# Optimization experiments

Hardware: AMD Instinct MI355X
Metric: run time of the kernel (lower is better)

Reference implementation:

```python
import jax, jax.numpy as jnp
import numpy as np

N_HEADS = 8
EMBED = 640
CROSS = 768
HEAD = EMBED // N_HEADS


def setup_inputs() -> dict:
    key = jax.random.key(0)
    ks = jax.random.split(key, 10)
    s_e = 1.0 / np.sqrt(EMBED)
    s_c = 1.0 / np.sqrt(CROSS)
    return {
        "x": jax.random.normal(ks[0], (8, 4096, EMBED), jnp.float32),
        "y": jax.random.normal(ks[1], (8, 77, CROSS), jnp.float32),
        "Wq": jax.random.uniform(ks[2], (EMBED, EMBED), jnp.float32, -s_e, s_e),
        "bq": jax.random.uniform(ks[3], (EMBED,), jnp.float32, -s_e, s_e),
        "Wk": jax.random.uniform(ks[4], (CROSS, EMBED), jnp.float32, -s_c, s_c),
        "bk": jax.random.uniform(ks[5], (EMBED,), jnp.float32, -s_c, s_c),
        "Wv": jax.random.uniform(ks[6], (CROSS, EMBED), jnp.float32, -s_c, s_c),
        "bv": jax.random.uniform(ks[7], (EMBED,), jnp.float32, -s_c, s_c),
        "Wo": jax.random.uniform(ks[8], (EMBED, EMBED), jnp.float32, -s_e, s_e),
        "bo": jax.random.uniform(ks[9], (EMBED,), jnp.float32, -s_e, s_e),
    }


def reference(x, y, Wq, bq, Wk, bk, Wv, bv, Wo, bo):
    B, T, C = x.shape
    S = y.shape[1]
    # projections; split heads: [B, H, T, D]
    q = (x @ Wq + bq).reshape(B, T, N_HEADS, HEAD).transpose(0, 2, 1, 3)
    k = (y @ Wk + bk).reshape(B, S, N_HEADS, HEAD).transpose(0, 2, 1, 3)
    v = (y @ Wv + bv).reshape(B, S, N_HEADS, HEAD).transpose(0, 2, 1, 3)
    scores = jnp.einsum("bhtd,bhsd->bhts", q, k) / jnp.sqrt(jnp.float32(HEAD))
    attn = jax.nn.softmax(scores, axis=-1)
    out = jnp.einsum("bhts,bhsd->bhtd", attn, v)
    out = out.transpose(0, 2, 1, 3).reshape(B, T, C)
    return out @ Wo + bo
```

## Files before the change

kernel.cpp:

```cpp
#include <hip/hip_runtime.h>
#include <hip/hip_bf16.h>
#include <hip/hip_fp16.h>

#define EMBED 640
#define CROSS 768
#define NH 8
#define HEAD 80
#define BATCH 8
#define SEQT 4096
#define SEQS 77
#define MROWS (BATCH * SEQT)

typedef _Float16 half8 __attribute__((ext_vector_type(8)));
typedef float floatx4 __attribute__((ext_vector_type(4)));

__device__ __forceinline__ void lds_load16(const void* g, void* l) {
    __builtin_amdgcn_global_load_lds(
        (const __attribute__((address_space(1))) void*)g,
        (__attribute__((address_space(3))) void*)l, 16, 0, 0);
}

__global__ __launch_bounds__(256) void cvt_f32_f16(
    const float* __restrict__ in, _Float16* __restrict__ out)
{
    size_t i = ((size_t)blockIdx.x * 256 + threadIdx.x) * 8;
    float4 a = *(const float4*)&in[i];
    float4 b = *(const float4*)&in[i + 4];
    half8 h;
    h[0] = (_Float16)a.x; h[1] = (_Float16)a.y;
    h[2] = (_Float16)a.z; h[3] = (_Float16)a.w;
    h[4] = (_Float16)b.x; h[5] = (_Float16)b.y;
    h[6] = (_Float16)b.z; h[7] = (_Float16)b.w;
    *(half8*)&out[i] = h;
}

__global__ __launch_bounds__(256) void cvt_y_f16(
    const float* __restrict__ y, _Float16* __restrict__ yh)
{
    size_t i = ((size_t)blockIdx.x * 256 + threadIdx.x) * 8;
    half8 h = {};
    if (i < (size_t)BATCH * SEQS * CROSS) {
        float4 a = *(const float4*)&y[i];
        float4 b = *(const float4*)&y[i + 4];
        h[0] = (_Float16)a.x; h[1] = (_Float16)a.y;
        h[2] = (_Float16)a.z; h[3] = (_Float16)a.w;
        h[4] = (_Float16)b.x; h[5] = (_Float16)b.y;
        h[6] = (_Float16)b.z; h[7] = (_Float16)b.w;
    }
    *(half8*)&yh[i] = h;
}

__global__ __launch_bounds__(256) void zero_f16(_Float16* __restrict__ p, size_t n8)
{
    size_t i = (size_t)blockIdx.x * 256 + threadIdx.x;
    if (i < n8) *(half8*)&p[i * 8] = (half8){};
}

__global__ __launch_bounds__(256) void transpose_cvt(
    const float* __restrict__ W, _Float16* __restrict__ Wt, int K, int N)
{
    __shared__ float t[32][33];
    const int k0 = blockIdx.y * 32, n0 = blockIdx.x * 32;
    for (int r = threadIdx.y; r < 32; r += 8)
        t[r][threadIdx.x] = W[(size_t)(k0 + r) * N + n0 + threadIdx.x];
    __syncthreads();
    for (int r = threadIdx.y; r < 32; r += 8)
        Wt[(size_t)(n0 + r) * K + k0 + threadIdx.x] = (_Float16)t[threadIdx.x][r];
}

template <bool HALF_OUT>
__global__ __launch_bounds__(256) void gemm_f16(
    const _Float16* __restrict__ A,
    const _Float16* __restrict__ Bt,
    const float* __restrict__ bias,
    void* __restrict__ Cout, int M, int N, int K, float scale)
{
    __shared__ _Float16 As[3][128 * 32];
    __shared__ _Float16 Bs[3][128 * 32];

    const int tid  = threadIdx.x;
    const int wave = tid >> 6;
    const int lane = tid & 63;
    const int quad = lane >> 4;
    const int l16  = lane & 15;

    const int l   = blockIdx.y * gridDim.x + blockIdx.x;
    const int inner = l >> 3;
    const int p   = (l & 7) + 8 * (inner / gridDim.x);
    const int nt  = inner % gridDim.x;
    const int m0 = p * 128, n0 = nt * 128;
    const int wm = (wave >> 1) * 64, wn = (wave & 1) * 64;

    const int row = tid >> 2;
    const int kch = ((tid & 3) ^ ((row >> 1) & 3)) * 8;
    const int cq  = (quad ^ ((l16 >> 1) & 3)) * 8;

    const _Float16* pa0 = &A [(size_t)(m0 + row)      * K + kch];
    const _Float16* pa1 = &A [(size_t)(m0 + 64 + row) * K + kch];
    const _Float16* pb0 = &Bt[(size_t)(n0 + row)      * K + kch];
    const _Float16* pb1 = &Bt[(size_t)(n0 + 64 + row) * K + kch];

    const int NT = K / 32;

    auto stage = [&](int t) {
        const int bf = t % 3;
        const int off = t * 32;
        lds_load16(pa0 + off, &As[bf][wave * 512]);
        lds_load16(pa1 + off, &As[bf][2048 + wave * 512]);
        lds_load16(pb0 + off, &Bs[bf][wave * 512]);
        lds_load16(pb1 + off, &Bs[bf][2048 + wave * 512]);
    };
    stage(0); stage(1); stage(2);

    floatx4 acc[4][4] = {};

    for (int t = 0; t < NT; ++t) {
        const int rem = NT - 1 - t;
        if (rem >= 2)      asm volatile("s_waitcnt vmcnt(8)" ::: "memory");
        else if (rem == 1) asm volatile("s_waitcnt vmcnt(4)" ::: "memory");
        else               asm volatile("s_waitcnt vmcnt(0)" ::: "memory");
        __builtin_amdgcn_s_barrier();

        const _Float16* as = As[t % 3];
        const _Float16* bs = Bs[t % 3];
        half8 a[4], b[4];
        #pragma unroll
        for (int i = 0; i < 4; ++i)
            a[i] = *(const half8*)&as[(wm + i * 16 + l16) * 32 + cq];
        #pragma unroll
        for (int j = 0; j < 4; ++j)
            b[j] = *(const half8*)&bs[(wn + j * 16 + l16) * 32 + cq];
        #pragma unroll
        for (int i = 0; i < 4; ++i)
            #pragma unroll
            for (int j = 0; j < 4; ++j)
                acc[i][j] = __builtin_amdgcn_mfma_f32_16x16x32_f16(
                    a[i], b[j], acc[i][j], 0, 0, 0);

        asm volatile("s_waitcnt lgkmcnt(0)" ::: "memory");
        __builtin_amdgcn_s_barrier();
        if (t + 3 < NT) stage(t + 3);
    }

    float bcol[4];
    #pragma unroll
    for (int j = 0; j < 4; ++j) bcol[j] = bias[n0 + wn + j * 16 + l16];
    #pragma unroll
    for (int i = 0; i < 4; ++i)
        #pragma unroll
        for (int r = 0; r < 4; ++r) {
            const int m = m0 + wm + i * 16 + quad * 4 + r;
            #pragma unroll
            for (int j = 0; j < 4; ++j) {
                float v = (acc[i][j][r] + bcol[j]) * scale;
                const size_t off = (size_t)m * N + n0 + wn + j * 16 + l16;
                if (HALF_OUT) ((_Float16*)Cout)[off] = (_Float16)v;
                else          ((float*)Cout)[off] = v;
            }
        }
}

__global__ __launch_bounds__(256) void kv_gemm(
    const _Float16* __restrict__ yh,
    const _Float16* __restrict__ Wkt, const _Float16* __restrict__ Wvt,
    const float* __restrict__ bk, const float* __restrict__ bv,
    _Float16* __restrict__ kh, _Float16* __restrict__ vth)
{
    __shared__ _Float16 As[64 * 32];
    __shared__ _Float16 Bs[64 * 32];

    const int tid = threadIdx.x;
    const int wave = tid >> 6, lane = tid & 63;
    const int quad = lane >> 4, l16 = lane & 15;
    const int m0 = blockIdx.y * 64, n0 = blockIdx.x * 64;
    const bool isV = blockIdx.z != 0;
    const _Float16* Bt = isV ? Wvt : Wkt;
    const float* bias  = isV ? bv : bk;

    const int row = tid >> 2;
    const int kch = (tid & 3) * 8;

    floatx4 acc[4] = {};

    for (int k0 = 0; k0 < CROSS; k0 += 32) {
        lds_load16(&yh[(size_t)(m0 + row) * CROSS + k0 + kch], &As[wave * 512]);
        lds_load16(&Bt[(size_t)(n0 + row) * CROSS + k0 + kch], &Bs[wave * 512]);
        __syncthreads();
        half8 b = *(const half8*)&Bs[(wave * 16 + l16) * 32 + quad * 8];
        #pragma unroll
        for (int i = 0; i < 4; ++i) {
            half8 a = *(const half8*)&As[(i * 16 + l16) * 32 + quad * 8];
            acc[i] = __builtin_amdgcn_mfma_f32_16x16x32_f16(a, b, acc[i], 0, 0, 0);
        }
        __syncthreads();
    }

    const int n = n0 + wave * 16 + l16;
    const int h = n / HEAD, d = n % HEAD;
    const float bb = bias[n];
    #pragma unroll
    for (int i = 0; i < 4; ++i)
        #pragma unroll
        for (int r = 0; r < 4; ++r) {
            const int m = m0 + i * 16 + quad * 4 + r;
            if (m >= BATCH * SEQS) continue;
            const int b_ = m / SEQS, s = m % SEQS;
            const int bh = b_ * NH + h;
            const float v = acc[i][r] + bb;
            if (isV) vth[(size_t)bh * (HEAD * 80) + d * 80 + s] = (_Float16)v;
            else     kh [(size_t)bh * (SEQS * HEAD) + s * HEAD + d] = (_Float16)v;
        }
}

__global__ __launch_bounds__(256, 4) void attn_mfma(
    const _Float16* __restrict__ qh,
    const _Float16* __restrict__ kh,
    const _Float16* __restrict__ vth,
    _Float16* __restrict__ oh)
{
    constexpr int LS = 88;
    __shared__ _Float16 lds[(80 + 80 + 64) * LS + 8];
    _Float16* Ks = lds;
    _Float16* Vt = lds + 80 * LS;
    _Float16* Ps = lds + 160 * LS;

    const int tid = threadIdx.x;
    const int wave = tid >> 6, lane = tid & 63;
    const int quad = lane >> 4, l16 = lane & 15;
    const int bh = blockIdx.y;
    const int b = bh >> 3, h = bh & 7;
    const size_t row0 = (size_t)b * SEQT + (size_t)blockIdx.x * 256;
    const half8 hz = {};

    const _Float16* qp = qh + (row0 + wave * 16 + l16) * EMBED + h * HEAD;

    half8 qa0 = *(const half8*)&qp[quad * 8];
    half8 qa1 = *(const half8*)&qp[32 + quad * 8];
    half8 qa2 = (quad < 2) ? *(const half8*)&qp[64 + quad * 8] : hz;

    for (int idx = tid; idx < 80 * 11; idx += 256) {
        const int s = idx / 11, c = idx % 11;
        half8 v = hz;
        if (s < SEQS && c < 10)
            v = *(const half8*)&kh[(size_t)bh * (SEQS * HEAD) + s * HEAD + c * 8];
        *(half8*)&Ks[s * LS + c * 8] = v;
    }
    for (int idx = tid; idx < 80 * 11; idx += 256) {
        const int d = idx / 11, c = idx % 11;
        half8 v = hz;
        if (c < 10)
            v = *(const half8*)&vth[(size_t)bh * (HEAD * 80) + d * 80 + c * 8];
        *(half8*)&Vt[d * LS + c * 8] = v;
    }
    __syncthreads();

    for (int t = 0; t < 4; ++t) {
        floatx4 accs[5] = {};
        #pragma unroll
        for (int st = 0; st < 5; ++st) {
            const _Float16* kr = &Ks[(st * 16 + l16) * LS];
            half8 b0 = *(const half8*)&kr[quad * 8];
            half8 b1 = *(const half8*)&kr[32 + quad * 8];
            half8 b2 = *(const half8*)&kr[64 + quad * 8];
            accs[st] = __builtin_amdgcn_mfma_f32_16x16x32_f16(qa0, b0, accs[st], 0, 0, 0);
            accs[st] = __builtin_amdgcn_mfma_f32_16x16x32_f16(qa1, b1, accs[st], 0, 0, 0);
            accs[st] = __builtin_amdgcn_mfma_f32_16x16x32_f16(qa2, b2, accs[st], 0, 0, 0);
        }
        if (l16 >= 13) {
            accs[4][0] = -1e30f; accs[4][1] = -1e30f;
            accs[4][2] = -1e30f; accs[4][3] = -1e30f;
        }

        float recip[4];
        #pragma unroll
        for (int r = 0; r < 4; ++r) {
            float m = accs[0][r];
            #pragma unroll
            for (int st = 1; st < 5; ++st) m = fmaxf(m, accs[st][r]);
            m = fmaxf(m, __shfl_xor(m, 1));
            m = fmaxf(m, __shfl_xor(m, 2));
            m = fmaxf(m, __shfl_xor(m, 4));
            m = fmaxf(m, __shfl_xor(m, 8));
            float l = 0.f;
            const int row = wave * 16 + quad * 4 + r;
            #pragma unroll
            for (int st = 0; st < 5; ++st) {
                float e = __expf(accs[st][r] - m);
                l += e;
                Ps[row * LS + st * 16 + l16] = (_Float16)e;
            }
            l += __shfl_xor(l, 1);
            l += __shfl_xor(l, 2);
            l += __shfl_xor(l, 4);
            l += __shfl_xor(l, 8);
            recip[r] = 1.0f / l;
        }
        __syncthreads();

        half8 qn0 = hz, qn1 = hz, qn2 = hz;
        if (t < 3) {
            const _Float16* qn = qp + (size_t)(t + 1) * 64 * EMBED;
            qn0 = *(const half8*)&qn[quad * 8];
            qn1 = *(const half8*)&qn[32 + quad * 8];
            if (quad < 2) qn2 = *(const half8*)&qn[64 + quad * 8];
        }

        const _Float16* pr = &Ps[(wave * 16 + l16) * LS];
        half8 pa0 = *(const half8*)&pr[quad * 8];
        half8 pa1 = *(const half8*)&pr[32 + quad * 8];
        half8 pa2 = (quad < 2) ? *(const half8*)&pr[64 + quad * 8] : hz;
        __syncthreads();

        floatx4 acco[5] = {};
        #pragma unroll
        for (int dt = 0; dt < 5; ++dt) {
            const _Float16* vr = &Vt[(dt * 16 + l16) * LS];
            half8 b0 = *(const half8*)&vr[quad * 8];
            half8 b1 = *(const half8*)&vr[32 + quad * 8];
            half8 b2 = *(const half8*)&vr[64 + quad * 8];
            acco[dt] = __builtin_amdgcn_mfma_f32_16x16x32_f16(pa0, b0, acco[dt], 0, 0, 0);
            acco[dt] = __builtin_amdgcn_mfma_f32_16x16x32_f16(pa1, b1, acco[dt], 0, 0, 0);
            acco[dt] = __builtin_amdgcn_mfma_f32_16x16x32_f16(pa2, b2, acco[dt], 0, 0, 0);
        }

        #pragma unroll
        for (int r = 0; r < 4; ++r) {
            const size_t grow = row0 + t * 64 + wave * 16 + quad * 4 + r;
            #pragma unroll
            for (int dt = 0; dt < 5; ++dt)
                oh[grow * EMBED + h * HEAD + dt * 16 + l16] =
                    (_Float16)(acco[dt][r] * recip[r]);
        }

        qa0 = qn0; qa1 = qn1; qa2 = qn2;
    }
}

extern "C" void kernel_launch(void* const* d_in, const int* in_sizes, int n_in,
                              void* d_out, int out_size, void* d_ws, size_t ws_size,
                              hipStream_t stream)
{
    const float* x  = (const float*)d_in[0];
    const float* y  = (const float*)d_in[1];
    const float* Wq = (const float*)d_in[2];
    const float* bq = (const float*)d_in[3];
    const float* Wk = (const float*)d_in[4];
    const float* bk = (const float*)d_in[5];
    const float* Wv = (const float*)d_in[6];
    const float* bv = (const float*)d_in[7];
    const float* Wo = (const float*)d_in[8];
    const float* bo = (const float*)d_in[9];
    float* out = (float*)d_out;

    const size_t ME = (size_t)MROWS * EMBED;
    _Float16* xh  = (_Float16*)d_ws;
    _Float16* qh  = xh + ME;
    _Float16* ah  = qh + ME;
    _Float16* kh  = ah + ME;
    _Float16* vth = kh  + (size_t)BATCH * NH * SEQS * HEAD;
    _Float16* wqt = vth + (size_t)BATCH * NH * HEAD * 80;
    _Float16* wot = wqt + (size_t)EMBED * EMBED;
    _Float16* yh  = wot + (size_t)EMBED * EMBED;
    _Float16* wkt = yh  + (size_t)640 * CROSS;
    _Float16* wvt = wkt + (size_t)EMBED * CROSS;

    cvt_f32_f16<<<dim3(ME / (256 * 8)), 256, 0, stream>>>(x, xh);
    transpose_cvt<<<dim3(EMBED / 32, EMBED / 32), dim3(32, 8), 0, stream>>>(Wq, wqt, EMBED, EMBED);
    transpose_cvt<<<dim3(EMBED / 32, EMBED / 32), dim3(32, 8), 0, stream>>>(Wo, wot, EMBED, EMBED);
    transpose_cvt<<<dim3(EMBED / 32, CROSS / 32), dim3(32, 8), 0, stream>>>(Wk, wkt, CROSS, EMBED);
    transpose_cvt<<<dim3(EMBED / 32, CROSS / 32), dim3(32, 8), 0, stream>>>(Wv, wvt, CROSS, EMBED);
    cvt_y_f16<<<dim3(640 * CROSS / (256 * 8)), 256, 0, stream>>>(y, yh);
    zero_f16<<<dim3(((size_t)BATCH * NH * HEAD * 80 / 8 + 255) / 256), 256, 0, stream>>>(
        vth, (size_t)BATCH * NH * HEAD * 80 / 8);

    gemm_f16<true><<<dim3(EMBED / 128, MROWS / 128), 256, 0, stream>>>(
        xh, wqt, bq, qh, MROWS, EMBED, EMBED, 0.11180339887498949f);
    kv_gemm<<<dim3(EMBED / 64, 640 / 64, 2), 256, 0, stream>>>(
        yh, wkt, wvt, bk, bv, kh, vth);
    attn_mfma<<<dim3(SEQT / 256, BATCH * NH), 256, 0, stream>>>(qh, kh, vth, ah);
    gemm_f16<false><<<dim3(EMBED / 128, MROWS / 128), 256, 0, stream>>>(
        ah, wot, bo, out, MROWS, EMBED, EMBED, 1.0f);
}
```

Baseline: 301.2 us.

## Merge setup kernels and use single-barrier prefetch pipeline in GEMM

Folds the four weight transposes into one launch indexed by blockIdx.z, and combines the y conversion with zeroing of the V buffer into another. This cuts the number of small kernel launches. The GEMM main loop now uses a prefetch depth of two and issues the next stage right after a single barrier, dropping the second barrier and lgkmcnt wait per iteration. The risk is less memory latency hiding with the shallower prefetch, and possible races if the three-buffer rotation does not fully protect a buffer still being read.

```diff
diff --git a/kernel.cpp b/kernel.cpp
--- a/kernel.cpp
+++ b/kernel.cpp
@@ -34,38 +34,50 @@
     *(half8*)&out[i] = h;
 }
 
-__global__ __launch_bounds__(256) void cvt_y_f16(
-    const float* __restrict__ y, _Float16* __restrict__ yh)
-{
-    size_t i = ((size_t)blockIdx.x * 256 + threadIdx.x) * 8;
-    half8 h = {};
-    if (i < (size_t)BATCH * SEQS * CROSS) {
-        float4 a = *(const float4*)&y[i];
-        float4 b = *(const float4*)&y[i + 4];
-        h[0] = (_Float16)a.x; h[1] = (_Float16)a.y;
-        h[2] = (_Float16)a.z; h[3] = (_Float16)a.w;
-        h[4] = (_Float16)b.x; h[5] = (_Float16)b.y;
-        h[6] = (_Float16)b.z; h[7] = (_Float16)b.w;
-    }
-    *(half8*)&yh[i] = h;
-}
-
-__global__ __launch_bounds__(256) void zero_f16(_Float16* __restrict__ p, size_t n8)
-{
-    size_t i = (size_t)blockIdx.x * 256 + threadIdx.x;
-    if (i < n8) *(half8*)&p[i * 8] = (half8){};
-}
-
-__global__ __launch_bounds__(256) void transpose_cvt(
-    const float* __restrict__ W, _Float16* __restrict__ Wt, int K, int N)
+__global__ __launch_bounds__(256) void transpose_all(
+    const float* __restrict__ Wq, const float* __restrict__ Wo,
+    const float* __restrict__ Wk, const float* __restrict__ Wv,
+    _Float16* __restrict__ wqt, _Float16* __restrict__ wot,
+    _Float16* __restrict__ wkt, _Float16* __restrict__ wvt)
 {
     __shared__ float t[32][33];
+    const int z = blockIdx.z;
+    const float* W;  _Float16* Wt;  int K;
+    if      (z == 0) { W = Wq; Wt = wqt; K = EMBED; }
+    else if (z == 1) { W = Wo; Wt = wot; K = EMBED; }
+    else if (z == 2) { W = Wk; Wt = wkt; K = CROSS; }
+    else             { W = Wv; Wt = wvt; K = CROSS; }
+    const int N = EMBED;
     const int k0 = blockIdx.y * 32, n0 = blockIdx.x * 32;
+    if (k0 >= K) return;
     for (int r = threadIdx.y; r < 32; r += 8)
         t[r][threadIdx.x] = W[(size_t)(k0 + r) * N + n0 + threadIdx.x];
     __syncthreads();
     for (int r = threadIdx.y; r < 32; r += 8)
         Wt[(size_t)(n0 + r) * K + k0 + threadIdx.x] = (_Float16)t[threadIdx.x][r];
+}
+
+__global__ __launch_bounds__(256) void cvt_y_zero(
+    const float* __restrict__ y, _Float16* __restrict__ yh,
+    _Float16* __restrict__ vth)
+{
+    const size_t i = (size_t)blockIdx.x * 256 + threadIdx.x;
+    if (i < (size_t)640 * CROSS / 8) {
+        const size_t e = i * 8;
+        half8 h = {};
+        if (e < (size_t)BATCH * SEQS * CROSS) {
+            float4 a = *(const float4*)&y[e];
+            float4 b = *(const float4*)&y[e + 4];
+            h[0] = (_Float16)a.x; h[1] = (_Float16)a.y;
+            h[2] = (_Float16)a.z; h[3] = (_Float16)a.w;
+            h[4] = (_Float16)b.x; h[5] = (_Float16)b.y;
+            h[6] = (_Float16)b.z; h[7] = (_Float16)b.w;
+        }
+        *(half8*)&yh[e] = h;
+    } else {
+        const size_t j = (i - (size_t)640 * CROSS / 8) * 8;
+        *(half8*)&vth[j] = (half8){};
+    }
 }
 
 template <bool HALF_OUT>
@@ -110,16 +122,15 @@
         lds_load16(pb0 + off, &Bs[bf][wave * 512]);
         lds_load16(pb1 + off, &Bs[bf][2048 + wave * 512]);
     };
-    stage(0); stage(1); stage(2);
+    stage(0); stage(1);
 
     floatx4 acc[4][4] = {};
 
     for (int t = 0; t < NT; ++t) {
-        const int rem = NT - 1 - t;
-        if (rem >= 2)      asm volatile("s_waitcnt vmcnt(8)" ::: "memory");
-        else if (rem == 1) asm volatile("s_waitcnt vmcnt(4)" ::: "memory");
-        else               asm volatile("s_waitcnt vmcnt(0)" ::: "memory");
+        if (t < NT - 1) asm volatile("s_waitcnt vmcnt(4)" ::: "memory");
+        else            asm volatile("s_waitcnt vmcnt(0)" ::: "memory");
         __builtin_amdgcn_s_barrier();
+        if (t + 2 < NT) stage(t + 2);
 
         const _Float16* as = As[t % 3];
         const _Float16* bs = Bs[t % 3];
@@ -136,10 +147,6 @@
             for (int j = 0; j < 4; ++j)
                 acc[i][j] = __builtin_amdgcn_mfma_f32_16x16x32_f16(
                     a[i], b[j], acc[i][j], 0, 0, 0);
-
-        asm volatile("s_waitcnt lgkmcnt(0)" ::: "memory");
-        __builtin_amdgcn_s_barrier();
-        if (t + 3 < NT) stage(t + 3);
     }
 
     float bcol[4];
@@ -364,14 +371,10 @@
     _Float16* wkt = yh  + (size_t)640 * CROSS;
     _Float16* wvt = wkt + (size_t)EMBED * CROSS;
 
+    transpose_all<<<dim3(EMBED / 32, CROSS / 32, 4), dim3(32, 8), 0, stream>>>(
+        Wq, Wo, Wk, Wv, wqt, wot, wkt, wvt);
+    cvt_y_zero<<<dim3(440), 256, 0, stream>>>(y, yh, vth);
     cvt_f32_f16<<<dim3(ME / (256 * 8)), 256, 0, stream>>>(x, xh);
-    transpose_cvt<<<dim3(EMBED / 32, EMBED / 32), dim3(32, 8), 0, stream>>>(Wq, wqt, EMBED, EMBED);
-    transpose_cvt<<<dim3(EMBED / 32, EMBED / 32), dim3(32, 8), 0, stream>>>(Wo, wot, EMBED, EMBED);
-    transpose_cvt<<<dim3(EMBED / 32, CROSS / 32), dim3(32, 8), 0, stream>>>(Wk, wkt, CROSS, EMBED);
-    transpose_cvt<<<dim3(EMBED / 32, CROSS / 32), dim3(32, 8), 0, stream>>>(Wv, wvt, CROSS, EMBED);
-    cvt_y_f16<<<dim3(640 * CROSS / (256 * 8)), 256, 0, stream>>>(y, yh);
-    zero_f16<<<dim3(((size_t)BATCH * NH * HEAD * 80 / 8 + 255) / 256), 256, 0, stream>>>(
-        vth, (size_t)BATCH * NH * HEAD * 80 / 8);
 
     gemm_f16<true><<<dim3(EMBED / 128, MROWS / 128), 256, 0, stream>>>(
         xh, wqt, bq, qh, MROWS, EMBED, EMBED, 0.11180339887498949f);
```

New measurement: 294.3 us. 2.3% less time.
